# Performance work log

Measured on AMD Instinct MI355X. Metric: run time of the kernel, lower is better.

## Reference

```python
import math
import jax, jax.numpy as jnp
import numpy as np

B, S, E = 2, 2048, 2048
H, D = 16, 128

def setup_inputs() -> dict:
    key = jax.random.key(0)
    ks = jax.random.split(key, 5)
    scale = 0.02
    return {
        "hidden_states": jax.random.normal(ks[0], (B, S, E), dtype=jnp.float32),
        "Wq": jax.random.normal(ks[1], (E, E), dtype=jnp.float32) * scale,
        "Wk": jax.random.normal(ks[2], (E, E), dtype=jnp.float32) * scale,
        "Wv": jax.random.normal(ks[3], (E, E), dtype=jnp.float32) * scale,
        "Wo": jax.random.normal(ks[4], (E, E), dtype=jnp.float32) * scale,
        "bo": jnp.zeros((E,), dtype=jnp.float32),
    }

def _split_heads(x):
    # [B,S,E] -> [B,H,S,D]
    b, s, _ = x.shape
    return x.reshape(b, s, H, D).transpose(0, 2, 1, 3)

def reference(hidden_states, Wq, Wk, Wv, Wo, bo):
    # torch nn.Linear: y = x @ W.T (q/k/v have no bias)
    q = _split_heads(hidden_states @ Wq.T)
    k = _split_heads(hidden_states @ Wk.T)
    v = _split_heads(hidden_states @ Wv.T)
    scores = jnp.einsum("bhqd,bhkd->bhqk", q, k) / math.sqrt(D)
    # causal mask: strictly-upper-triangular positions set to -inf ...
    causal = jnp.triu(jnp.ones((S, S), dtype=bool), k=1)
    scores = jnp.where(causal[None, None], -jnp.inf, scores)
    # ... then clamped to [-1e4, 1e4] (so masked logits become -10000, not -inf)
    scores = jnp.clip(scores, -10000.0, 10000.0)
    attn = jax.nn.softmax(scores, axis=-1)
    out = jnp.einsum("bhqk,bhkd->bhqd", attn, v)  # [B,H,S,D]
    out = out.transpose(0, 2, 1, 3).reshape(B, S, E)  # merge heads
    return out @ Wo.T + bo
```

## Files before the change

kernel.cpp:

```cpp
#include <hip/hip_runtime.h>
#include <hip/hip_bf16.h>
#include <stdint.h>
#include <math.h>

#define B_ 2
#define S_ 2048
#define E_ 2048
#define H_ 16
#define D_ 128
#define M_ (B_*S_)

typedef _Float16 half8 __attribute__((ext_vector_type(8)));
typedef _Float16 half4 __attribute__((ext_vector_type(4)));
typedef float    floatx4 __attribute__((ext_vector_type(4)));

__device__ __forceinline__ void async_copy16(const void* g, void* lds_base) {
    __builtin_amdgcn_global_load_lds(
        (__attribute__((address_space(1))) void*)(uintptr_t)g,
        (__attribute__((address_space(3))) void*)(uint32_t)(uintptr_t)lds_base,
        16, 0, 0);
}

__global__ __launch_bounds__(256) void cast_all(
    const float* __restrict__ X,  const float* __restrict__ Wq,
    const float* __restrict__ Wk, const float* __restrict__ Wv,
    const float* __restrict__ Wo,
    _Float16* __restrict__ Xh,  _Float16* __restrict__ Wqh,
    _Float16* __restrict__ Wkh, _Float16* __restrict__ Wvh,
    _Float16* __restrict__ Woh)
{
    const int z = blockIdx.z;
    const float* in; _Float16* out; int n4;
    const int ME4 = M_*E_/4, EE4 = E_*E_/4;
    switch (z) {
        case 0: in = X;  out = Xh;  n4 = ME4; break;
        case 1: in = Wq; out = Wqh; n4 = EE4; break;
        case 2: in = Wk; out = Wkh; n4 = EE4; break;
        case 3: in = Wv; out = Wvh; n4 = EE4; break;
        default: in = Wo; out = Woh; n4 = EE4; break;
    }
    int i = blockIdx.x * 256 + threadIdx.x;
    if (i < n4) {
        floatx4 v = ((const floatx4*)in)[i];
        ((half4*)out)[i] = __builtin_convertvector(v, half4);
    }
}

#define GBUF (128*64 + 256*64)

__device__ __forceinline__ void stage512(
    const _Float16* __restrict__ gsrc, int ldk,
    _Float16* lbase, int slot0, int wave, int lane)
{
    int slot = slot0 + wave*64 + lane;
    int row  = slot >> 3;
    int sg   = (slot & 7) ^ (row & 7);
    async_copy16(gsrc + (size_t)row * ldk + sg * 8,
                 lbase + (slot0 + wave*64) * 8);
}

template<bool BIAS, typename OutT, int NW>
__global__ __launch_bounds__(512, 2) void gemm_bt(
    const _Float16* __restrict__ A,
    const _Float16* __restrict__ W0, const _Float16* __restrict__ W1,
    const _Float16* __restrict__ W2,
    OutT* __restrict__ C0, OutT* __restrict__ C1, OutT* __restrict__ C2,
    const float* __restrict__ bias, int M, int N, int K)
{
    const _Float16* W = W0; OutT* C = C0;
    if (NW > 1) {
        if (blockIdx.y == 1) { W = W1; C = C1; }
        else if (blockIdx.y == 2) { W = W2; C = C2; }
    }
    __shared__ __align__(16) _Float16 sm[3 * GBUF];

    const int tid  = threadIdx.x;
    const int lane = tid & 63;
    const int wave = tid >> 6;
    const int wm = wave >> 2, wn = wave & 3;
    const int fr = lane & 15, fg = lane >> 4;

    const int bx = blockIdx.x;
    const int n_tile = bx & 7;
    const int m_tile = bx >> 3;
    const int m0 = m_tile * 128;
    const int n0 = n_tile * 256;

    const int NT = K >> 6;

#pragma unroll
    for (int pt = 0; pt < 2; ++pt) {
        _Float16* ab = &sm[pt * GBUF];
        _Float16* bb = ab + 128*64;
        const _Float16* Ag = A + (size_t)m0 * K + pt*64;
        const _Float16* Wg = W + (size_t)n0 * K + pt*64;
        stage512(Ag, K, ab, 0,    wave, lane);
        stage512(Ag, K, ab, 512,  wave, lane);
        stage512(Wg, K, bb, 0,    wave, lane);
        stage512(Wg, K, bb, 512,  wave, lane);
        stage512(Wg, K, bb, 1024, wave, lane);
        stage512(Wg, K, bb, 1536, wave, lane);
    }

    floatx4 acc[4][4] = {};

    for (int t = 0; t < NT; ++t) {
        if (t + 1 < NT) { __asm__ __volatile__("s_waitcnt vmcnt(6)" ::: "memory"); }
        else            { __asm__ __volatile__("s_waitcnt vmcnt(0)" ::: "memory"); }
        __builtin_amdgcn_sched_barrier(0);
        __builtin_amdgcn_s_barrier();
        __builtin_amdgcn_sched_barrier(0);

        const _Float16* Ab = &sm[(t % 3) * GBUF];
        const _Float16* Bb = Ab + 128*64;
        const bool pf = (t + 2 < NT);
        _Float16* pab = &sm[((t + 2) % 3) * GBUF];
        _Float16* pbb = pab + 128*64;
        const _Float16* pAg = A + (size_t)m0 * K + (t + 2)*64;
        const _Float16* pWg = W + (size_t)n0 * K + (t + 2)*64;

        half8 af[4][2], bf[4][2];
#pragma unroll
        for (int mt = 0; mt < 4; ++mt)
#pragma unroll
            for (int kk = 0; kk < 2; ++kk) {
                int row = wm*64 + mt*16 + fr;
                int g = (kk*4 + fg) ^ (row & 7);
                af[mt][kk] = *(const half8*)&Ab[row*64 + g*8];
            }
#pragma unroll
        for (int nt = 0; nt < 4; ++nt)
#pragma unroll
            for (int kk = 0; kk < 2; ++kk) {
                int row = wn*64 + nt*16 + fr;
                int g = (kk*4 + fg) ^ (row & 7);
                bf[nt][kk] = *(const half8*)&Bb[row*64 + g*8];
            }

        if (pf) {
            stage512(pAg, K, pab, 0,    wave, lane);
            stage512(pAg, K, pab, 512,  wave, lane);
            stage512(pWg, K, pbb, 0,    wave, lane);
            stage512(pWg, K, pbb, 512,  wave, lane);
            stage512(pWg, K, pbb, 1024, wave, lane);
            stage512(pWg, K, pbb, 1536, wave, lane);
        }

        __builtin_amdgcn_s_setprio(1);
#pragma unroll
        for (int kk = 0; kk < 2; ++kk)
#pragma unroll
            for (int nt = 0; nt < 4; ++nt)
#pragma unroll
                for (int mt = 0; mt < 4; ++mt)
                    acc[mt][nt] = __builtin_amdgcn_mfma_f32_16x16x32_f16(
                        af[mt][kk], bf[nt][kk], acc[mt][nt], 0, 0, 0);
        __builtin_amdgcn_s_setprio(0);
    }

#pragma unroll
    for (int mt = 0; mt < 4; ++mt)
#pragma unroll
        for (int nt = 0; nt < 4; ++nt) {
            int col = n0 + wn*64 + nt*16 + fr;
            float bv = BIAS ? bias[col] : 0.f;
#pragma unroll
            for (int r = 0; r < 4; ++r) {
                int row = m0 + wm*64 + mt*16 + fg*4 + r;
                C[(size_t)row * N + col] = (OutT)(acc[mt][nt][r] + bv);
            }
        }
}

__global__ __launch_bounds__(256) void transpose_v(
    const _Float16* __restrict__ V, _Float16* __restrict__ Vt)
{
    __shared__ __align__(16) _Float16 t[64][72];
    const int bh = blockIdx.z;
    const int b = bh >> 4, h = bh & 15;
    const int s0 = blockIdx.x * 64, d0 = blockIdx.y * 64;
    const int tid = threadIdx.x;
#pragma unroll
    for (int i = 0; i < 2; ++i) {
        int e = (i*256 + tid) * 8;
        int row = e >> 6, col = e & 63;
        *(half8*)&t[row][col] =
            *(const half8*)&V[(size_t)(b*S_ + s0 + row) * E_ + h*D_ + d0 + col];
    }
    __syncthreads();
#pragma unroll
    for (int i = 0; i < 2; ++i) {
        int e = (i*256 + tid) * 8;
        int dr = e >> 6, col = e & 63;
        half8 v;
#pragma unroll
        for (int j = 0; j < 8; ++j) v[j] = t[col + j][dr];
        *(half8*)&Vt[((size_t)bh * D_ + d0 + dr) * S_ + s0 + col] = v;
    }
}

__global__ __launch_bounds__(256, 2) void attn_causal_coop(
    const _Float16* __restrict__ Q, const _Float16* __restrict__ K,
    const _Float16* __restrict__ Vt, _Float16* __restrict__ O)
{
    const int n   = blockIdx.x;
    const int xcd = n & 7;
    const int idx = n >> 3;
    const int bh  = xcd * 4 + (idx >> 4);
    const int j   = idx & 15;
    const int b = bh >> 4, h = bh & 15;
    const int tid = threadIdx.x, lane = tid & 63, wave = tid >> 6;
    const int fr = lane & 15, fg = lane >> 4;

    __shared__ __align__(16) _Float16 Ks[64*128];
    __shared__ __align__(16) _Float16 Vs[128*64];
    __shared__ __align__(16) _Float16 Ps[4][32*72];

    const int rhi = (31 - j) * 64 + wave * 16;
    const int rlo = j * 64 + wave * 16;
    const int nkt = 32 - j;

    half8 qf[2][4];
    {
        const _Float16* qb0 = Q + ((size_t)(b*S_) + rhi) * E_ + h*D_;
        const _Float16* qb1 = Q + ((size_t)(b*S_) + rlo) * E_ + h*D_;
#pragma unroll
        for (int kk = 0; kk < 4; ++kk) {
            qf[0][kk] = *(const half8*)&qb0[(size_t)fr * E_ + kk*32 + fg*8];
            qf[1][kk] = *(const half8*)&qb1[(size_t)fr * E_ + kk*32 + fg*8];
        }
    }

    float m_i[2][4], l_i[2][4];
    floatx4 o[2][8] = {};
#pragma unroll
    for (int mt = 0; mt < 2; ++mt)
#pragma unroll
        for (int r = 0; r < 4; ++r) { m_i[mt][r] = -INFINITY; l_i[mt][r] = 0.f; }

    const float scale = 0.088388347648318447f;
    const _Float16* kg = K + (size_t)(b*S_) * E_ + h*D_;
    const _Float16* vg = Vt + (size_t)bh * D_ * S_;
    _Float16* ps = &Ps[wave][0];

    for (int jt = 0; jt < nkt; ++jt) {
        __syncthreads();
#pragma unroll
        for (int q = 0; q < 4; ++q) {
            int G = q*256 + tid;
            int row = G >> 4, slot = G & 15;
            int c = slot ^ (row & 7);
            async_copy16(kg + (size_t)(jt*64 + row) * E_ + c*8,
                         &Ks[(q*256 + wave*64) * 8]);
        }
#pragma unroll
        for (int q = 0; q < 4; ++q) {
            int G = q*256 + tid;
            int row = G >> 3, slot = G & 7;
            int c = slot ^ (row & 7);
            async_copy16(vg + (size_t)row * S_ + jt*64 + c*8,
                         &Vs[(q*256 + wave*64) * 8]);
        }
        __syncthreads();

        const bool lo_act = (jt <= j);

        floatx4 sacc[2][4] = {};
#pragma unroll
        for (int kk = 0; kk < 4; ++kk) {
            half8 bf[4];
#pragma unroll
            for (int nt = 0; nt < 4; ++nt)
                bf[nt] = *(const half8*)
                    &Ks[(nt*16 + fr)*128 + (((kk*4 + fg) ^ (fr & 7)) * 8)];
#pragma unroll
            for (int nt = 0; nt < 4; ++nt)
                sacc[0][nt] = __builtin_amdgcn_mfma_f32_16x16x32_f16(
                    qf[0][kk], bf[nt], sacc[0][nt], 0, 0, 0);
            if (lo_act) {
#pragma unroll
                for (int nt = 0; nt < 4; ++nt)
                    sacc[1][nt] = __builtin_amdgcn_mfma_f32_16x16x32_f16(
                        qf[1][kk], bf[nt], sacc[1][nt], 0, 0, 0);
            }
        }

        const int kc0 = jt*64 + fr;
#pragma unroll
        for (int mt = 0; mt < 2; ++mt) {
            if (mt == 1 && !lo_act) continue;
            const int qr0 = (mt ? rlo : rhi) + fg*4;
            float alpha[4];
#pragma unroll
            for (int r = 0; r < 4; ++r) {
                float mx = -INFINITY;
#pragma unroll
                for (int nt = 0; nt < 4; ++nt) {
                    float s = sacc[mt][nt][r] * scale;
                    s = (kc0 + nt*16 <= qr0 + r) ? s : -INFINITY;
                    sacc[mt][nt][r] = s;
                    mx = fmaxf(mx, s);
                }
                mx = fmaxf(mx, __shfl_xor(mx, 1));
                mx = fmaxf(mx, __shfl_xor(mx, 2));
                mx = fmaxf(mx, __shfl_xor(mx, 4));
                mx = fmaxf(mx, __shfl_xor(mx, 8));
                float mnew = fmaxf(m_i[mt][r], mx);
                alpha[r] = (m_i[mt][r] == -INFINITY) ? 0.f : __expf(m_i[mt][r] - mnew);
                float rs = 0.f;
#pragma unroll
                for (int nt = 0; nt < 4; ++nt) {
                    float p = __expf(sacc[mt][nt][r] - mnew);
                    sacc[mt][nt][r] = p;
                    rs += p;
                }
                rs += __shfl_xor(rs, 1);
                rs += __shfl_xor(rs, 2);
                rs += __shfl_xor(rs, 4);
                rs += __shfl_xor(rs, 8);
                l_i[mt][r] = alpha[r] * l_i[mt][r] + rs;
                m_i[mt][r] = mnew;
            }
#pragma unroll
            for (int dt = 0; dt < 8; ++dt)
#pragma unroll
                for (int r = 0; r < 4; ++r) o[mt][dt][r] *= alpha[r];

#pragma unroll
            for (int nt = 0; nt < 4; ++nt)
#pragma unroll
                for (int r = 0; r < 4; ++r)
                    ps[(mt*16 + fg*4 + r)*72 + nt*16 + fr] = (_Float16)sacc[mt][nt][r];
        }
        __asm__ __volatile__("s_waitcnt lgkmcnt(0)" ::: "memory");

#pragma unroll
        for (int kk = 0; kk < 2; ++kk) {
            half8 pf0 = *(const half8*)&ps[(fr)*72 + kk*32 + fg*8];
            half8 pf1 = *(const half8*)&ps[(16 + fr)*72 + kk*32 + fg*8];
#pragma unroll
            for (int dt = 0; dt < 8; ++dt) {
                half8 vf = *(const half8*)
                    &Vs[(dt*16 + fr)*64 + (((kk*4 + fg) ^ (fr & 7)) * 8)];
                o[0][dt] = __builtin_amdgcn_mfma_f32_16x16x32_f16(
                    pf0, vf, o[0][dt], 0, 0, 0);
                if (lo_act)
                    o[1][dt] = __builtin_amdgcn_mfma_f32_16x16x32_f16(
                        pf1, vf, o[1][dt], 0, 0, 0);
            }
        }
    }

#pragma unroll
    for (int mt = 0; mt < 2; ++mt) {
        const int rbase = mt ? rlo : rhi;
        _Float16* ob = O + ((size_t)(b*S_) + rbase) * E_ + h*D_;
#pragma unroll
        for (int r = 0; r < 4; ++r) {
            float inv = 1.f / l_i[mt][r];
#pragma unroll
            for (int dt = 0; dt < 8; ++dt)
                ob[(size_t)(fg*4 + r) * E_ + dt*16 + fr] = (_Float16)(o[mt][dt][r] * inv);
        }
    }
}

extern "C" void kernel_launch(void* const* d_in, const int* in_sizes, int n_in,
                              void* d_out, int out_size, void* d_ws, size_t ws_size,
                              hipStream_t stream) {
    const float* X  = (const float*)d_in[0];
    const float* Wq = (const float*)d_in[1];
    const float* Wk = (const float*)d_in[2];
    const float* Wv = (const float*)d_in[3];
    const float* Wo = (const float*)d_in[4];
    const float* bo = (const float*)d_in[5];
    float* out = (float*)d_out;

    const size_t ME = (size_t)M_ * E_;
    const size_t EE = (size_t)E_ * E_;
    _Float16* ws  = (_Float16*)d_ws;
    _Float16* Xh  = ws;
    _Float16* Wqh = Xh  + ME;
    _Float16* Wkh = Wqh + EE;
    _Float16* Wvh = Wkh + EE;
    _Float16* Woh = Wvh + EE;
    _Float16* Qh  = Woh + EE;
    _Float16* Kh  = Qh  + ME;
    _Float16* Vh  = Kh  + ME;
    _Float16* Vth = Xh;
    _Float16* Oh  = Vh;

    cast_all<<<dim3(ME/4/256, 1, 5), dim3(256), 0, stream>>>(
        X, Wq, Wk, Wv, Wo, Xh, Wqh, Wkh, Wvh, Woh);

    gemm_bt<false, _Float16, 3><<<dim3(256, 3), dim3(512), 0, stream>>>(
        Xh, Wqh, Wkh, Wvh, Qh, Kh, Vh, nullptr, M_, E_, E_);

    transpose_v<<<dim3(S_/64, D_/64, B_*H_), dim3(256), 0, stream>>>(Vh, Vth);

    attn_causal_coop<<<dim3(512), dim3(256), 0, stream>>>(Qh, Kh, Vth, Oh);

    gemm_bt<true, float, 1><<<dim3(256, 1), dim3(512), 0, stream>>>(
        Oh, Woh, nullptr, nullptr, out, nullptr, nullptr, bo, M_, E_, E_);
}
```

Baseline: 385.1 us.

## Fuse V transpose into QKV GEMM epilogue and double-buffer K tiles in attention

```diff
diff --git a/kernel.cpp b/kernel.cpp
--- a/kernel.cpp
+++ b/kernel.cpp
@@ -30,20 +30,18 @@
     _Float16* __restrict__ Woh)
 {
     const int z = blockIdx.z;
-    const float* in; _Float16* out; int n4;
-    const int ME4 = M_*E_/4, EE4 = E_*E_/4;
+    const float* in; _Float16* out; size_t off = 0;
     switch (z) {
-        case 0: in = X;  out = Xh;  n4 = ME4; break;
-        case 1: in = Wq; out = Wqh; n4 = EE4; break;
-        case 2: in = Wk; out = Wkh; n4 = EE4; break;
-        case 3: in = Wv; out = Wvh; n4 = EE4; break;
-        default: in = Wo; out = Woh; n4 = EE4; break;
-    }
-    int i = blockIdx.x * 256 + threadIdx.x;
-    if (i < n4) {
-        floatx4 v = ((const floatx4*)in)[i];
-        ((half4*)out)[i] = __builtin_convertvector(v, half4);
-    }
+        case 0: in = X;  out = Xh;  off = 0;        break;
+        case 1: in = X;  out = Xh;  off = 1048576;  break;
+        case 2: in = Wq; out = Wqh; break;
+        case 3: in = Wk; out = Wkh; break;
+        case 4: in = Wv; out = Wvh; break;
+        default: in = Wo; out = Woh; break;
+    }
+    size_t i = off + (size_t)blockIdx.x * 256 + threadIdx.x;
+    floatx4 v = ((const floatx4*)in)[i];
+    ((half4*)out)[i] = __builtin_convertvector(v, half4);
 }
 
 #define GBUF (128*64 + 256*64)
@@ -59,7 +57,7 @@
                  lbase + (slot0 + wave*64) * 8);
 }
 
-template<bool BIAS, typename OutT, int NW>
+template<bool BIAS, typename OutT, int NW, bool TRV>
 __global__ __launch_bounds__(512, 2) void gemm_bt(
     const _Float16* __restrict__ A,
     const _Float16* __restrict__ W0, const _Float16* __restrict__ W1,
@@ -158,44 +156,34 @@
         __builtin_amdgcn_s_setprio(0);
     }
 
-#pragma unroll
-    for (int mt = 0; mt < 4; ++mt)
-#pragma unroll
-        for (int nt = 0; nt < 4; ++nt) {
-            int col = n0 + wn*64 + nt*16 + fr;
-            float bv = BIAS ? bias[col] : 0.f;
-#pragma unroll
-            for (int r = 0; r < 4; ++r) {
-                int row = m0 + wm*64 + mt*16 + fg*4 + r;
-                C[(size_t)row * N + col] = (OutT)(acc[mt][nt][r] + bv);
-            }
-        }
-}
-
-__global__ __launch_bounds__(256) void transpose_v(
-    const _Float16* __restrict__ V, _Float16* __restrict__ Vt)
-{
-    __shared__ __align__(16) _Float16 t[64][72];
-    const int bh = blockIdx.z;
-    const int b = bh >> 4, h = bh & 15;
-    const int s0 = blockIdx.x * 64, d0 = blockIdx.y * 64;
-    const int tid = threadIdx.x;
-#pragma unroll
-    for (int i = 0; i < 2; ++i) {
-        int e = (i*256 + tid) * 8;
-        int row = e >> 6, col = e & 63;
-        *(half8*)&t[row][col] =
-            *(const half8*)&V[(size_t)(b*S_ + s0 + row) * E_ + h*D_ + d0 + col];
-    }
-    __syncthreads();
-#pragma unroll
-    for (int i = 0; i < 2; ++i) {
-        int e = (i*256 + tid) * 8;
-        int dr = e >> 6, col = e & 63;
-        half8 v;
-#pragma unroll
-        for (int j = 0; j < 8; ++j) v[j] = t[col + j][dr];
-        *(half8*)&Vt[((size_t)bh * D_ + d0 + dr) * S_ + s0 + col] = v;
+    if (TRV && NW > 1 && blockIdx.y == 2) {
+        _Float16* Vt = (_Float16*)C;
+#pragma unroll
+        for (int mt = 0; mt < 4; ++mt)
+#pragma unroll
+            for (int nt = 0; nt < 4; ++nt) {
+                int col  = n0 + wn*64 + nt*16 + fr;
+                int row0 = m0 + wm*64 + mt*16 + fg*4;
+                int bq = row0 >> 11, s0 = row0 & 2047;
+                int hq = col >> 7,  dq = col & 127;
+                half4 v;
+#pragma unroll
+                for (int r = 0; r < 4; ++r) v[r] = (_Float16)acc[mt][nt][r];
+                *(half4*)&Vt[(((size_t)(bq*16 + hq) * 128 + dq) << 11) + s0] = v;
+            }
+    } else {
+#pragma unroll
+        for (int mt = 0; mt < 4; ++mt)
+#pragma unroll
+            for (int nt = 0; nt < 4; ++nt) {
+                int col = n0 + wn*64 + nt*16 + fr;
+                float bv = BIAS ? bias[col] : 0.f;
+#pragma unroll
+                for (int r = 0; r < 4; ++r) {
+                    int row = m0 + wm*64 + mt*16 + fg*4 + r;
+                    C[(size_t)row * N + col] = (OutT)(acc[mt][nt][r] + bv);
+                }
+            }
     }
 }
 
@@ -212,7 +200,7 @@
     const int tid = threadIdx.x, lane = tid & 63, wave = tid >> 6;
     const int fr = lane & 15, fg = lane >> 4;
 
-    __shared__ __align__(16) _Float16 Ks[64*128];
+    __shared__ __align__(16) _Float16 Ks[2][64*128];
     __shared__ __align__(16) _Float16 Vs[128*64];
     __shared__ __align__(16) _Float16 Ps[4][32*72];
 
@@ -243,16 +231,20 @@
     const _Float16* vg = Vt + (size_t)bh * D_ * S_;
     _Float16* ps = &Ps[wave][0];
 
+#pragma unroll
+    for (int q = 0; q < 4; ++q) {
+        int G = q*256 + tid;
+        int row = G >> 4, slot = G & 15;
+        int c = slot ^ (row & 7);
+        async_copy16(kg + (size_t)row * E_ + c*8, &Ks[0][(q*256 + wave*64) * 8]);
+    }
+
     for (int jt = 0; jt < nkt; ++jt) {
-        __syncthreads();
-#pragma unroll
-        for (int q = 0; q < 4; ++q) {
-            int G = q*256 + tid;
-            int row = G >> 4, slot = G & 15;
-            int c = slot ^ (row & 7);
-            async_copy16(kg + (size_t)(jt*64 + row) * E_ + c*8,
-                         &Ks[(q*256 + wave*64) * 8]);
-        }
+        __asm__ __volatile__("s_waitcnt vmcnt(0)" ::: "memory");
+        __builtin_amdgcn_sched_barrier(0);
+        __builtin_amdgcn_s_barrier();
+        __builtin_amdgcn_sched_barrier(0);
+
 #pragma unroll
         for (int q = 0; q < 4; ++q) {
             int G = q*256 + tid;
@@ -261,18 +253,30 @@
             async_copy16(vg + (size_t)row * S_ + jt*64 + c*8,
                          &Vs[(q*256 + wave*64) * 8]);
         }
-        __syncthreads();
+        const bool pk = (jt + 1 < nkt);
+        if (pk) {
+#pragma unroll
+            for (int q = 0; q < 4; ++q) {
+                int G = q*256 + tid;
+                int row = G >> 4, slot = G & 15;
+                int c = slot ^ (row & 7);
+                async_copy16(kg + (size_t)((jt+1)*64 + row) * E_ + c*8,
+                             &Ks[(jt+1) & 1][(q*256 + wave*64) * 8]);
+            }
+        }
 
         const bool lo_act = (jt <= j);
+        const _Float16* kt = &Ks[jt & 1][0];
 
         floatx4 sacc[2][4] = {};
+        __builtin_amdgcn_s_setprio(1);
 #pragma unroll
         for (int kk = 0; kk < 4; ++kk) {
             half8 bf[4];
 #pragma unroll
             for (int nt = 0; nt < 4; ++nt)
                 bf[nt] = *(const half8*)
-                    &Ks[(nt*16 + fr)*128 + (((kk*4 + fg) ^ (fr & 7)) * 8)];
+                    &kt[(nt*16 + fr)*128 + (((kk*4 + fg) ^ (fr & 7)) * 8)];
 #pragma unroll
             for (int nt = 0; nt < 4; ++nt)
                 sacc[0][nt] = __builtin_amdgcn_mfma_f32_16x16x32_f16(
@@ -284,6 +288,7 @@
                         qf[1][kk], bf[nt], sacc[1][nt], 0, 0, 0);
             }
         }
+        __builtin_amdgcn_s_setprio(0);
 
         const int kc0 = jt*64 + fr;
 #pragma unroll
@@ -333,7 +338,15 @@
                     ps[(mt*16 + fg*4 + r)*72 + nt*16 + fr] = (_Float16)sacc[mt][nt][r];
         }
         __asm__ __volatile__("s_waitcnt lgkmcnt(0)" ::: "memory");
-
+        __builtin_amdgcn_sched_barrier(0);
+
+        if (pk) { __asm__ __volatile__("s_waitcnt vmcnt(4)" ::: "memory"); }
+        else    { __asm__ __volatile__("s_waitcnt vmcnt(0)" ::: "memory"); }
+        __builtin_amdgcn_sched_barrier(0);
+        __builtin_amdgcn_s_barrier();
+        __builtin_amdgcn_sched_barrier(0);
+
+        __builtin_amdgcn_s_setprio(1);
 #pragma unroll
         for (int kk = 0; kk < 2; ++kk) {
             half8 pf0 = *(const half8*)&ps[(fr)*72 + kk*32 + fg*8];
@@ -349,6 +362,7 @@
                         pf1, vf, o[1][dt], 0, 0, 0);
             }
         }
+        __builtin_amdgcn_s_setprio(0);
     }
 
 #pragma unroll
@@ -386,20 +400,17 @@
     _Float16* Woh = Wvh + EE;
     _Float16* Qh  = Woh + EE;
     _Float16* Kh  = Qh  + ME;
-    _Float16* Vh  = Kh  + ME;
-    _Float16* Vth = Xh;
-    _Float16* Oh  = Vh;
-
-    cast_all<<<dim3(ME/4/256, 1, 5), dim3(256), 0, stream>>>(
+    _Float16* Vth = Kh  + ME;
+    _Float16* Oh  = Xh;
+
+    cast_all<<<dim3(4096, 1, 6), dim3(256), 0, stream>>>(
         X, Wq, Wk, Wv, Wo, Xh, Wqh, Wkh, Wvh, Woh);
 
-    gemm_bt<false, _Float16, 3><<<dim3(256, 3), dim3(512), 0, stream>>>(
-        Xh, Wqh, Wkh, Wvh, Qh, Kh, Vh, nullptr, M_, E_, E_);
-
-    transpose_v<<<dim3(S_/64, D_/64, B_*H_), dim3(256), 0, stream>>>(Vh, Vth);
+    gemm_bt<false, _Float16, 3, true><<<dim3(256, 3), dim3(512), 0, stream>>>(
+        Xh, Wqh, Wkh, Wvh, Qh, Kh, Vth, nullptr, M_, E_, E_);
 
     attn_causal_coop<<<dim3(512), dim3(256), 0, stream>>>(Qh, Kh, Vth, Oh);
 
-    gemm_bt<true, float, 1><<<dim3(256, 1), dim3(512), 0, stream>>>(
+    gemm_bt<true, float, 1, false><<<dim3(256, 1), dim3(512), 0, stream>>>(
         Oh, Woh, nullptr, nullptr, out, nullptr, nullptr, bo, M_, E_, E_);
 }
```

Result: slower. 400.5 us (+4.0%).
